# Performance work log

Measured on AMD Instinct MI355X. Metric: run time of the kernel, lower is better.

## Reference

```python
import jax, jax.numpy as jnp
import numpy as np

B, LQ, LKV = 4, 512, 8192
Q_DIM, KV_DIM = 1024, 512
QK_CH, V_CH, N_HEADS = 256, 256, 8
EPS = 1e-5


def _layernorm(x, g, b):
    m = jnp.mean(x, axis=-1, keepdims=True)
    v = jnp.mean(jnp.square(x - m), axis=-1, keepdims=True)
    return (x - m) * jax.lax.rsqrt(v + EPS) * g + b


def setup_inputs() -> dict:
    key = jax.random.key(0)
    ks = jax.random.split(key, 8)
    hidden_states = jax.random.normal(ks[0], (B, LQ, Q_DIM), dtype=jnp.float32)
    inputs = jax.random.normal(ks[1], (B, LKV, KV_DIM), dtype=jnp.float32)
    # Linear weights stored as [in, out] for x @ W
    Wq = jax.random.normal(ks[2], (Q_DIM, QK_CH), dtype=jnp.float32) * (1.0 / np.sqrt(Q_DIM))
    Wk = jax.random.normal(ks[3], (KV_DIM, QK_CH), dtype=jnp.float32) * (1.0 / np.sqrt(KV_DIM))
    Wv = jax.random.normal(ks[4], (KV_DIM, V_CH), dtype=jnp.float32) * (1.0 / np.sqrt(KV_DIM))
    bq = jnp.zeros((QK_CH,), jnp.float32)
    bk = jax.random.normal(ks[5], (QK_CH,), dtype=jnp.float32) * 0.02
    bv = jax.random.normal(ks[6], (V_CH,), dtype=jnp.float32) * 0.02
    ln1_g = jnp.ones((Q_DIM,), jnp.float32)
    ln1_b = jnp.zeros((Q_DIM,), jnp.float32)
    ln2_g = jnp.ones((KV_DIM,), jnp.float32)
    ln2_b = jnp.zeros((KV_DIM,), jnp.float32)
    return dict(hidden_states=hidden_states, inputs=inputs,
                ln1_g=ln1_g, ln1_b=ln1_b, ln2_g=ln2_g, ln2_b=ln2_b,
                Wq=Wq, bq=bq, Wk=Wk, bk=bk, Wv=Wv, bv=bv)


def reference(hidden_states, inputs, ln1_g, ln1_b, ln2_g, ln2_b,
              Wq, bq, Wk, bk, Wv, bv):
    H = N_HEADS
    dqk = QK_CH // H
    dv = V_CH // H
    hs = _layernorm(hidden_states, ln1_g, ln1_b)          # [B,LQ,Q_DIM]
    inp = _layernorm(inputs, ln2_g, ln2_b)                # [B,LKV,KV_DIM]
    q = (hs @ Wq + bq).reshape(B, LQ, H, dqk)             # [B,LQ,H,dqk]
    k = (inp @ Wk + bk).reshape(B, LKV, H, dqk)           # [B,LKV,H,dqk]
    v = (inp @ Wv + bv).reshape(B, LKV, H, dv)            # [B,LKV,H,dv]
    scores = jnp.einsum('bqhd,bkhd->bhqk', q, k) / np.sqrt(dqk).astype(np.float32)
    probs = jax.nn.softmax(scores, axis=-1)               # [B,H,LQ,LKV] (materialized, as in torch)
    ctx = jnp.einsum('bhqk,bkhd->bqhd', probs, v)         # [B,LQ,H,dv]
    return ctx.reshape(B, LQ, H * dv)
```

## Files before the change

kernel.cpp:

```cpp
#include <hip/hip_runtime.h>
#include <hip/hip_bf16.h>
#include <math.h>

#define NB    4
#define LQ    512
#define LKV   8192
#define QDIM  1024
#define KVDIM 512
#define NH    8
#define EPS_LN 1e-5f
#define SMAX  12.0f

typedef __attribute__((ext_vector_type(8))) short bf16x8;
typedef __attribute__((ext_vector_type(4))) float f32x4;

static __device__ __forceinline__ ushort f2bf(float x) {
    unsigned int u = __builtin_bit_cast(unsigned int, x);
    u += 0x7FFFu + ((u >> 16) & 1u);
    return (ushort)(u >> 16);
}

#if __has_builtin(__builtin_amdgcn_cvt_pk_bf16_f32)
static __device__ __forceinline__ unsigned int pk_bf16(float a, float b) {
    auto r = __builtin_amdgcn_cvt_pk_bf16_f32(a, b);
    return __builtin_bit_cast(unsigned int, r);
}
#else
static __device__ __forceinline__ unsigned int pk_bf16(float a, float b) {
    return (unsigned int)f2bf(a) | ((unsigned int)f2bf(b) << 16);
}
#endif

#if __has_builtin(__builtin_amdgcn_exp2f)
#define EXP2F(x) __builtin_amdgcn_exp2f(x)
#else
#define EXP2F(x) exp2f(x)
#endif

static __device__ __forceinline__ void interleave_swap(unsigned int &x, unsigned int &y, int lane) {
#if __has_builtin(__builtin_amdgcn_permlane32_swap) && __has_builtin(__builtin_amdgcn_permlane16_swap)
    {
        auto r1 = __builtin_amdgcn_permlane32_swap(x, y, false, false);
        auto r2 = __builtin_amdgcn_permlane16_swap(r1[0], r1[1], false, false);
        x = (unsigned int)r2[0];
        y = (unsigned int)r2[1];
    }
#else
    {
        unsigned int xs = (unsigned int)__shfl_xor((int)x, 32, 64);
        unsigned int ys = (unsigned int)__shfl_xor((int)y, 32, 64);
        unsigned int A2 = (lane & 32) ? ys : x;
        unsigned int C2 = (lane & 32) ? y  : xs;
        unsigned int A2x = (unsigned int)__shfl_xor((int)A2, 16, 64);
        unsigned int C2x = (unsigned int)__shfl_xor((int)C2, 16, 64);
        x = (lane & 16) ? C2x : A2;
        y = (lane & 16) ? C2  : A2x;
    }
#endif
}

static __device__ __forceinline__ void gld_lds16(const ushort* g, ushort* l) {
    __builtin_amdgcn_global_load_lds(
        (const __attribute__((address_space(1))) unsigned int*)g,
        (__attribute__((address_space(3))) unsigned int*)l, 16, 0, 0);
}

template<int K>
static __device__ __forceinline__ void ln_norm_row(
    const float* __restrict__ x, const float* __restrict__ g,
    const float* __restrict__ bta, ushort* __restrict__ y, int row, int lane)
{
    const float* xp = x + (size_t)row * K;
    constexpr int NV = K / 256;
    float4 v[NV];
    float s = 0.f;
#pragma unroll
    for (int i = 0; i < NV; ++i) {
        v[i] = *(const float4*)(xp + lane * 4 + i * 256);
        s += v[i].x + v[i].y + v[i].z + v[i].w;
    }
#pragma unroll
    for (int o = 1; o < 64; o <<= 1) s += __shfl_xor(s, o, 64);
    const float mu = s * (1.0f / K);
    float vs = 0.f;
#pragma unroll
    for (int i = 0; i < NV; ++i) {
        float dx = v[i].x - mu, dy = v[i].y - mu, dz = v[i].z - mu, dw = v[i].w - mu;
        vs += dx * dx + dy * dy + dz * dz + dw * dw;
    }
#pragma unroll
    for (int o = 1; o < 64; o <<= 1) vs += __shfl_xor(vs, o, 64);
    const float rs = rsqrtf(vs * (1.0f / K) + EPS_LN);
#pragma unroll
    for (int i = 0; i < NV; ++i) {
        const float4 gv = *(const float4*)(g   + lane * 4 + i * 256);
        const float4 bv = *(const float4*)(bta + lane * 4 + i * 256);
        uint2 o;
        o.x = pk_bf16((v[i].x - mu) * rs * gv.x + bv.x, (v[i].y - mu) * rs * gv.y + bv.y);
        o.y = pk_bf16((v[i].z - mu) * rs * gv.z + bv.z, (v[i].w - mu) * rs * gv.w + bv.w);
        *(uint2*)(y + (size_t)row * K + lane * 4 + i * 256) = o;
    }
}

static __device__ __forceinline__ void ln_stats_row(
    const float* __restrict__ x, float* __restrict__ mean, float* __restrict__ rstd,
    int row, int lane)
{
    const float* xp = x + (size_t)row * QDIM;
    float4 v[4];
    float s = 0.f;
#pragma unroll
    for (int i = 0; i < 4; ++i) {
        v[i] = *(const float4*)(xp + lane * 4 + i * 256);
        s += v[i].x + v[i].y + v[i].z + v[i].w;
    }
#pragma unroll
    for (int o = 1; o < 64; o <<= 1) s += __shfl_xor(s, o, 64);
    const float mu = s * (1.0f / QDIM);
    float vs = 0.f;
#pragma unroll
    for (int i = 0; i < 4; ++i) {
        float dx = v[i].x - mu, dy = v[i].y - mu, dz = v[i].z - mu, dw = v[i].w - mu;
        vs += dx * dx + dy * dy + dz * dz + dw * dw;
    }
#pragma unroll
    for (int o = 1; o < 64; o <<= 1) vs += __shfl_xor(vs, o, 64);
    if (lane == 0) {
        mean[row] = mu;
        rstd[row] = rsqrtf(vs * (1.0f / QDIM) + EPS_LN);
    }
}

static __device__ __forceinline__ void wt_transpose_body(
    const float* __restrict__ src, ushort* __restrict__ dst, int K,
    int kx, int ny, int t, ushort (*Ts)[72])
{
    const int k0 = kx * 64, n0 = ny * 64;
    const int nl = t & 63;
#pragma unroll
    for (int p = 0; p < 16; ++p) {
        const int kl = p * 4 + (t >> 6);
        Ts[nl][kl] = f2bf(src[(size_t)(k0 + kl) * 256 + n0 + nl]);
    }
    __syncthreads();
    const int ck = (t & 7) * 8;
#pragma unroll
    for (int p = 0; p < 2; ++p) {
        const int rn = p * 32 + (t >> 3);
        *(bf16x8*)(dst + (size_t)(n0 + rn) * K + k0 + ck) = *(const bf16x8*)&Ts[rn][ck];
    }
}

__global__ __launch_bounds__(256) void phaseA_kernel(
    const float* __restrict__ inputs, const float* __restrict__ ln2g,
    const float* __restrict__ ln2b,   ushort* __restrict__ Abf,
    const float* __restrict__ hidden, float* __restrict__ mean_h, float* __restrict__ rstd_h,
    const float* __restrict__ Wq, const float* __restrict__ Wk, const float* __restrict__ Wv,
    ushort* __restrict__ WtQ, ushort* __restrict__ WtKV)
{
    __shared__ ushort Ts[64][72];
    const int bid = blockIdx.x;
    const int t = threadIdx.x;
    const int lane = t & 63;
    if (bid < 8192) {
        ln_norm_row<KVDIM>(inputs, ln2g, ln2b, Abf, bid * 4 + (t >> 6), lane);
    } else if (bid < 8704) {
        ln_stats_row(hidden, mean_h, rstd_h, (bid - 8192) * 4 + (t >> 6), lane);
    } else if (bid < 8768) {
        const int p = bid - 8704;
        wt_transpose_body(Wq, WtQ, QDIM, p & 15, p >> 4, t, Ts);
    } else if (bid < 8800) {
        const int p = bid - 8768;
        wt_transpose_body(Wk, WtKV, KVDIM, p & 7, p >> 3, t, Ts);
    } else {
        const int p = bid - 8800;
        wt_transpose_body(Wv, WtKV + (size_t)256 * KVDIM, KVDIM, p & 7, p >> 3, t, Ts);
    }
}

__global__ __launch_bounds__(256) void phaseB_kernel(
    const ushort* __restrict__ Abf, const ushort* __restrict__ WtKV,
    const float* __restrict__ bk, const float* __restrict__ bv,
    ushort* __restrict__ kb, ushort* __restrict__ vt,
    const float* __restrict__ hidden, const float* __restrict__ mean_h,
    const float* __restrict__ rstd_h,
    const float* __restrict__ ln1g, const float* __restrict__ ln1b,
    const ushort* __restrict__ WtQ, const float* __restrict__ bq,
    ushort* __restrict__ qb, float oscale)
{
    __shared__ __align__(16) ushort SMEM[4 * 64 * 72];
    const int bid  = blockIdx.x;
    const int t    = threadIdx.x;
    const int lane = t & 63;
    const int w    = t >> 6;
    const int lq   = lane & 15;
    const int lg   = lane >> 4;
    const int wm   = w >> 1;
    const int wn   = w & 1;

    if (bid < 1024) {
        const int bm = (bid >> 2) * 128;
        const int bn = (bid & 3) * 128;
        ushort* As = SMEM;
        ushort* Bs = SMEM + 4096;

        const int srow = t >> 2;
        const int scol = ((t & 3) ^ ((t >> 3) & 3)) * 8;
        const ushort* gA = Abf  + (size_t)(bm + srow) * KVDIM + scol;
        const ushort* gB = WtKV + (size_t)(bn + srow) * KVDIM + scol;
        ushort* lA = As + t * 8;
        ushort* lB = Bs + t * 8;

        f32x4 acc[4][4] = {};
        for (int k0 = 0; k0 < KVDIM; k0 += 32) {
            gld_lds16(gA + k0,                       lA);
            gld_lds16(gA + (size_t)64 * KVDIM + k0,  lA + 2048);
            gld_lds16(gB + k0,                       lB);
            gld_lds16(gB + (size_t)64 * KVDIM + k0,  lB + 2048);
            __syncthreads();
            bf16x8 af[4], bf[4];
#pragma unroll
            for (int mt = 0; mt < 4; ++mt) {
                const int m = wm * 64 + mt * 16 + lq;
                af[mt] = *(const bf16x8*)(As + m * 32 + ((lg ^ ((m >> 1) & 3)) << 3));
            }
#pragma unroll
            for (int nt = 0; nt < 4; ++nt) {
                const int n = wn * 64 + nt * 16 + lq;
                bf[nt] = *(const bf16x8*)(Bs + n * 32 + ((lg ^ ((n >> 1) & 3)) << 3));
            }
#pragma unroll
            for (int mt = 0; mt < 4; ++mt)
#pragma unroll
                for (int nt = 0; nt < 4; ++nt)
                    acc[mt][nt] = __builtin_amdgcn_mfma_f32_16x16x32_bf16(af[mt], bf[nt], acc[mt][nt], 0, 0, 0);
            __syncthreads();
        }
        const int m0base = bm + wm * 64;
        const int bidx   = m0base >> 13;
        const int tokb   = m0base & 8191;

        if (bn < 256) {
            ushort (*Cs)[72] = (ushort(*)[72])(SMEM + w * 64 * 72);
#pragma unroll
            for (int nt = 0; nt < 4; ++nt) {
                const int n_l = nt * 16 + lq;
                const float bias = bk[bn + wn * 64 + n_l];
#pragma unroll
                for (int mt = 0; mt < 4; ++mt)
#pragma unroll
                    for (int r = 0; r < 4; ++r)
                        Cs[mt * 16 + lg * 4 + r][n_l] = f2bf(acc[mt][nt][r] + bias);
            }
            const int r0 = lane >> 3;
            const int ck = (lane & 7) * 8;
            const int nc = bn + wn * 64 + ck;
            const int h = nc >> 5, d = nc & 31;
            const size_t obase = (((size_t)(bidx * NH + h) << 13) + tokb) * 32 + d;
#pragma unroll
            for (int p = 0; p < 8; ++p) {
                const int row = p * 8 + r0;
                *(bf16x8*)(kb + obase + (size_t)row * 32) = *(const bf16x8*)&Cs[row][ck];
            }
        } else {
            ushort (*Cs)[72] = (ushort(*)[72])(SMEM + w * 64 * 72);
#pragma unroll
            for (int nt = 0; nt < 4; ++nt) {
                const int n_l = nt * 16 + lq;
                const float bias = bv[(bn - 256) + wn * 64 + n_l];
#pragma unroll
                for (int mt = 0; mt < 4; ++mt) {
                    uint2 o;
                    o.x = pk_bf16(acc[mt][nt][0] + bias, acc[mt][nt][1] + bias);
                    o.y = pk_bf16(acc[mt][nt][2] + bias, acc[mt][nt][3] + bias);
                    *(uint2*)&Cs[n_l][mt * 16 + lg * 4] = o;
                }
            }
            const int r0 = lane >> 3;
            const int cm = (lane & 7) * 8;
            const int tokc = tokb + cm;
#pragma unroll
            for (int p = 0; p < 8; ++p) {
                const int row = p * 8 + r0;
                const int nv  = (bn - 256) + wn * 64 + row;
                const int h = nv >> 5, d = nv & 31;
                *(bf16x8*)(vt + ((size_t)(bidx * NH + h) * 32 + d) * LKV + tokc) =
                    *(const bf16x8*)&Cs[row][cm];
            }
        }
    } else {
        const int p  = bid - 1024;
        const int bm = (p >> 2) * 64;
        const int bn = (p & 3) * 64;
        ushort* As = SMEM;
        ushort* Bs = SMEM + 4096;

        const int srow = t >> 3;
        const int scol = ((t & 7) ^ (srow & 7)) * 8;
        const ushort* gB = WtQ + (size_t)(bn + srow) * QDIM + scol;
        ushort* lB  = Bs + t * 8;
        ushort* lA0 = As + t * 8;
        ushort* lA1 = As + 2048 + t * 8;

        const int r0 = bm + srow;
        const float mu0 = mean_h[r0],      rs0 = rstd_h[r0];
        const float mu1 = mean_h[r0 + 32], rs1 = rstd_h[r0 + 32];
        const float* xA0 = hidden + (size_t)r0 * QDIM + scol;
        const float* xA1 = xA0 + (size_t)32 * QDIM;

        f32x4 acc[2][2] = {};
        for (int k0 = 0; k0 < QDIM; k0 += 64) {
            gld_lds16(gB + k0,                      lB);
            gld_lds16(gB + (size_t)32 * QDIM + k0,  lB + 2048);
            const float4 a0 = *(const float4*)(xA0 + k0);
            const float4 a1 = *(const float4*)(xA0 + k0 + 4);
            const float4 c0 = *(const float4*)(xA1 + k0);
            const float4 c1 = *(const float4*)(xA1 + k0 + 4);
            const float4 g0 = *(const float4*)(ln1g + k0 + scol);
            const float4 g1 = *(const float4*)(ln1g + k0 + scol + 4);
            const float4 d0 = *(const float4*)(ln1b + k0 + scol);
            const float4 d1 = *(const float4*)(ln1b + k0 + scol + 4);
            uint4 w0, w1;
            w0.x = pk_bf16((a0.x - mu0) * rs0 * g0.x + d0.x, (a0.y - mu0) * rs0 * g0.y + d0.y);
            w0.y = pk_bf16((a0.z - mu0) * rs0 * g0.z + d0.z, (a0.w - mu0) * rs0 * g0.w + d0.w);
            w0.z = pk_bf16((a1.x - mu0) * rs0 * g1.x + d1.x, (a1.y - mu0) * rs0 * g1.y + d1.y);
            w0.w = pk_bf16((a1.z - mu0) * rs0 * g1.z + d1.z, (a1.w - mu0) * rs0 * g1.w + d1.w);
            w1.x = pk_bf16((c0.x - mu1) * rs1 * g0.x + d0.x, (c0.y - mu1) * rs1 * g0.y + d0.y);
            w1.y = pk_bf16((c0.z - mu1) * rs1 * g0.z + d0.z, (c0.w - mu1) * rs1 * g0.w + d0.w);
            w1.z = pk_bf16((c1.x - mu1) * rs1 * g1.x + d1.x, (c1.y - mu1) * rs1 * g1.y + d1.y);
            w1.w = pk_bf16((c1.z - mu1) * rs1 * g1.z + d1.z, (c1.w - mu1) * rs1 * g1.w + d1.w);
            *(uint4*)lA0 = w0;
            *(uint4*)lA1 = w1;
            __syncthreads();
#pragma unroll
            for (int kh = 0; kh < 2; ++kh) {
                bf16x8 af[2], bf[2];
#pragma unroll
                for (int mt = 0; mt < 2; ++mt) {
                    const int m = wm * 32 + mt * 16 + lq;
                    af[mt] = *(const bf16x8*)(As + m * 64 + (((lg + 4 * kh) ^ (m & 7)) << 3));
                }
#pragma unroll
                for (int nt = 0; nt < 2; ++nt) {
                    const int n = wn * 32 + nt * 16 + lq;
                    bf[nt] = *(const bf16x8*)(Bs + n * 64 + (((lg + 4 * kh) ^ (n & 7)) << 3));
                }
#pragma unroll
                for (int mt = 0; mt < 2; ++mt)
#pragma unroll
                    for (int nt = 0; nt < 2; ++nt)
                        acc[mt][nt] = __builtin_amdgcn_mfma_f32_16x16x32_bf16(af[mt], bf[nt], acc[mt][nt], 0, 0, 0);
            }
            __syncthreads();
        }

#pragma unroll
        for (int nt = 0; nt < 2; ++nt) {
            const int n = bn + wn * 32 + nt * 16 + lq;
            const int h = n >> 5, d = n & 31;
            const float bias = bq[n];
#pragma unroll
            for (int mt = 0; mt < 2; ++mt) {
                const int m0   = bm + wm * 32 + mt * 16 + lg * 4;
                const int bidx = m0 >> 9;
                const int tok  = m0 & 511;
                const size_t base = (((size_t)(bidx * NH + h) << 9) + tok) * 32 + d;
#pragma unroll
                for (int r = 0; r < 4; ++r)
                    qb[base + (size_t)r * 32] = f2bf((acc[mt][nt][r] + bias) * oscale);
            }
        }
    }
}

__global__ __launch_bounds__(256, 4) void attn_mfma_kernel(
    const ushort* __restrict__ Qb,
    const ushort* __restrict__ Kb,
    const ushort* __restrict__ Vt,
    float* __restrict__ Opart,
    float* __restrict__ lpart)
{
    const int bid = blockIdx.x;
    const int xcd = bid & 7;
    const int rr  = bid >> 3;
    const int bh  = ((rr & 3) << 3) | xcd;
    const int qt  = (rr >> 2) & 15;
    const int quarter = rr >> 6;
    const int t = threadIdx.x, w = t >> 6, lane = t & 63;
    const int lq = lane & 15, lg = lane >> 4;

    __shared__ __align__(16) float Ob[2 * 32 * 36];
    __shared__ float lbuf[4][32];

    bf16x8 qfrag[2];
    const size_t qbase = ((size_t)bh * LQ + qt * 32) * 32;
    qfrag[0] = *(const bf16x8*)(Qb + qbase + (size_t)lq * 32 + lg * 8);
    qfrag[1] = *(const bf16x8*)(Qb + qbase + (size_t)(16 + lq) * 32 + lg * 8);

    const int kv0 = quarter * 2048 + w * 512;
    const ushort* KpA = Kb + ((size_t)bh * LKV + kv0 + lq) * 32 + lg * 8;
    const ushort* VpA = Vt + ((size_t)bh * 32 + lq) * LKV + kv0 + lg * 8;

    f32x4 oacc[2][2] = {};
    float l_part[2] = {0.f, 0.f};
    const f32x4 cM = {-SMAX, -SMAX, -SMAX, -SMAX};

    bf16x8 kf[4];
#pragma unroll
    for (int m = 0; m < 4; ++m)
        kf[m] = *(const bf16x8*)(KpA + (size_t)(m * 16) * 32);

    for (int kt = 0; kt < 512; kt += 64) {
        bf16x8 kc[4];
#pragma unroll
        for (int m = 0; m < 4; ++m) kc[m] = kf[m];

        bf16x8 vc[2][2];
#pragma unroll
        for (int dt = 0; dt < 2; ++dt)
#pragma unroll
            for (int hf = 0; hf < 2; ++hf)
                vc[dt][hf] = *(const bf16x8*)(VpA + (size_t)(dt * 16) * LKV + kt + hf * 32);

        const int nk = (kt + 64 < 512) ? kt + 64 : 0;
#pragma unroll
        for (int m = 0; m < 4; ++m)
            kf[m] = *(const bf16x8*)(KpA + (size_t)(nk + m * 16) * 32);

        f32x4 s[4][2];
#pragma unroll
        for (int m = 0; m < 4; ++m)
#pragma unroll
            for (int n = 0; n < 2; ++n)
                s[m][n] = __builtin_amdgcn_mfma_f32_16x16x32_bf16(kc[m], qfrag[n], cM, 0, 0, 0);

        bf16x8 pf[2][2];
#pragma unroll
        for (int n = 0; n < 2; ++n) {
#pragma unroll
            for (int z = 0; z < 2; ++z) {
                const float e0 = EXP2F(s[2 * z][n][0]);
                const float e1 = EXP2F(s[2 * z][n][1]);
                const float e2 = EXP2F(s[2 * z][n][2]);
                const float e3 = EXP2F(s[2 * z][n][3]);
                const float f0 = EXP2F(s[2 * z + 1][n][0]);
                const float f1 = EXP2F(s[2 * z + 1][n][1]);
                const float f2 = EXP2F(s[2 * z + 1][n][2]);
                const float f3 = EXP2F(s[2 * z + 1][n][3]);
                l_part[n] += ((e0 + e1) + (e2 + e3)) + ((f0 + f1) + (f2 + f3));
                unsigned int wa = pk_bf16(e0, e1);
                unsigned int wb = pk_bf16(e2, e3);
                unsigned int wc = pk_bf16(f0, f1);
                unsigned int wd = pk_bf16(f2, f3);
                interleave_swap(wa, wc, lane);
                interleave_swap(wb, wd, lane);
                uint4 wv;
                wv.x = wa; wv.y = wb; wv.z = wc; wv.w = wd;
                pf[n][z] = __builtin_bit_cast(bf16x8, wv);
            }
        }

#pragma unroll
        for (int dt = 0; dt < 2; ++dt)
#pragma unroll
            for (int n = 0; n < 2; ++n) {
                oacc[dt][n] = __builtin_amdgcn_mfma_f32_16x16x32_bf16(vc[dt][0], pf[n][0], oacc[dt][n], 0, 0, 0);
                oacc[dt][n] = __builtin_amdgcn_mfma_f32_16x16x32_bf16(vc[dt][1], pf[n][1], oacc[dt][n], 0, 0, 0);
            }
    }

#pragma unroll
    for (int n = 0; n < 2; ++n) {
        l_part[n] += __shfl_xor(l_part[n], 16);
        l_part[n] += __shfl_xor(l_part[n], 32);
    }
    if (lg == 0) {
        lbuf[w][lq]      = l_part[0];
        lbuf[w][16 + lq] = l_part[1];
    }
    if (w >= 2) {
#pragma unroll
        for (int n = 0; n < 2; ++n)
#pragma unroll
            for (int dt = 0; dt < 2; ++dt)
                *(f32x4*)&Ob[((size_t)(w - 2) * 32 + n * 16 + lq) * 36 + dt * 16 + lg * 4] = oacc[dt][n];
    }
    __syncthreads();
    if (w < 2) {
#pragma unroll
        for (int n = 0; n < 2; ++n)
#pragma unroll
            for (int dt = 0; dt < 2; ++dt) {
                float* p = &Ob[((size_t)w * 32 + n * 16 + lq) * 36 + dt * 16 + lg * 4];
                f32x4 v = *(f32x4*)p;
                v += oacc[dt][n];
                *(f32x4*)p = v;
            }
    }
    __syncthreads();
    {
        const int pidx = (quarter * 32 + bh) * 16 + qt;
        const int q  = t >> 3;
        const int d0 = (t & 7) * 4;
        f32x4 s0 = *(const f32x4*)&Ob[((size_t)q) * 36 + d0];
        f32x4 s1 = *(const f32x4*)&Ob[((size_t)(32 + q)) * 36 + d0];
        s0 += s1;
        *(f32x4*)(Opart + (size_t)pidx * 1024 + q * 32 + d0) = s0;
        if ((t & 7) == 0) {
            float gl = lbuf[0][q] + lbuf[1][q] + lbuf[2][q] + lbuf[3][q];
            lpart[(size_t)pidx * 32 + q] = gl;
        }
    }
}

__global__ __launch_bounds__(256) void attn_combine_kernel(
    const float* __restrict__ Opart, const float* __restrict__ lpart,
    float* __restrict__ Out)
{
    const int cb = blockIdx.x;
    const int bh = cb >> 4, qt = cb & 15;
    const int b = bh >> 3, h = bh & 7;
    const int t = threadIdx.x;
    const int q = t >> 3;
    const int dq = (t & 7) * 4;
    float4 o = {0.f, 0.f, 0.f, 0.f};
    float l = 0.f;
#pragma unroll
    for (int j = 0; j < 4; ++j) {
        const size_t pidx = (size_t)((j * 32 + bh) * 16 + qt);
        const float4 a = *(const float4*)(Opart + pidx * 1024 + q * 32 + dq);
        o.x += a.x; o.y += a.y; o.z += a.z; o.w += a.w;
        l += lpart[pidx * 32 + q];
    }
    const float inv = 1.0f / l;
    o.x *= inv; o.y *= inv; o.z *= inv; o.w *= inv;
    *(float4*)(Out + ((size_t)b * LQ + qt * 32 + q) * 256 + h * 32 + dq) = o;
}

extern "C" void kernel_launch(void* const* d_in, const int* in_sizes, int n_in,
                              void* d_out, int out_size, void* d_ws, size_t ws_size,
                              hipStream_t stream)
{
    const float* hidden = (const float*)d_in[0];
    const float* inputs = (const float*)d_in[1];
    const float* ln1g   = (const float*)d_in[2];
    const float* ln1b   = (const float*)d_in[3];
    const float* ln2g   = (const float*)d_in[4];
    const float* ln2b   = (const float*)d_in[5];
    const float* Wq     = (const float*)d_in[6];
    const float* bq     = (const float*)d_in[7];
    const float* Wk     = (const float*)d_in[8];
    const float* bk     = (const float*)d_in[9];
    const float* Wv     = (const float*)d_in[10];
    const float* bv     = (const float*)d_in[11];
    float* out = (float*)d_out;

    char* wsb = (char*)d_ws;
    ushort* qb     = (ushort*)(wsb);
    ushort* WtKV   = (ushort*)(wsb + (1u << 20));
    ushort* WtQ    = (ushort*)(wsb + (1u << 20) + (512u << 10));
    float*  mean_h = (float*)(wsb + (2u << 20));
    float*  rstd_h = (float*)(wsb + (2u << 20) + 8192);
    ushort* kb     = (ushort*)(wsb + (2u << 20) + 16384);
    ushort* vt     = (ushort*)(wsb + (18u << 20) + 16384);
    ushort* Abf    = (ushort*)(wsb + (34u << 20) + 16384);

    float* Opart = (float*)Abf;
    float* lpart = Opart + (size_t)4 * 32 * 16 * 1024;

    const float oscale = 0.2550540226496112f;

    phaseA_kernel<<<8832, 256, 0, stream>>>(inputs, ln2g, ln2b, Abf,
                                            hidden, mean_h, rstd_h,
                                            Wq, Wk, Wv, WtQ, WtKV);
    phaseB_kernel<<<1152, 256, 0, stream>>>(Abf, WtKV, bk, bv, kb, vt,
                                            hidden, mean_h, rstd_h, ln1g, ln1b,
                                            WtQ, bq, qb, oscale);
    attn_mfma_kernel<<<2048, 256, 0, stream>>>(qb, kb, vt, Opart, lpart);
    attn_combine_kernel<<<512, 256, 0, stream>>>(Opart, lpart, out);
}
```

Baseline: 219.0 us.

## Double K-step of KV projection GEMM and reorder attention block mapping

The KV projection GEMM now loads a 64-wide K slice per iteration instead of 32, halving the number of loop iterations and barrier pairs. It uses an 8-way XOR swizzle adapted to the 64-element row stride. Separately, the attention kernel's block-index decode is reordered so consecutive blocks on an XCD share the same batch-head, which should improve L2 locality for K/V. The price is doubled LDS use for the GEMM tiles, which could lower occupancy.

```diff
diff --git a/kernel.cpp b/kernel.cpp
--- a/kernel.cpp
+++ b/kernel.cpp
@@ -202,38 +202,40 @@
         const int bm = (bid >> 2) * 128;
         const int bn = (bid & 3) * 128;
         ushort* As = SMEM;
-        ushort* Bs = SMEM + 4096;
-
-        const int srow = t >> 2;
-        const int scol = ((t & 3) ^ ((t >> 3) & 3)) * 8;
+        ushort* Bs = SMEM + 8192;
+
+        const int srow = t >> 3;
+        const int scol = ((t & 7) ^ (srow & 7)) * 8;
         const ushort* gA = Abf  + (size_t)(bm + srow) * KVDIM + scol;
         const ushort* gB = WtKV + (size_t)(bn + srow) * KVDIM + scol;
-        ushort* lA = As + t * 8;
-        ushort* lB = Bs + t * 8;
 
         f32x4 acc[4][4] = {};
-        for (int k0 = 0; k0 < KVDIM; k0 += 32) {
-            gld_lds16(gA + k0,                       lA);
-            gld_lds16(gA + (size_t)64 * KVDIM + k0,  lA + 2048);
-            gld_lds16(gB + k0,                       lB);
-            gld_lds16(gB + (size_t)64 * KVDIM + k0,  lB + 2048);
+        for (int k0 = 0; k0 < KVDIM; k0 += 64) {
+#pragma unroll
+            for (int p = 0; p < 4; ++p) {
+                gld_lds16(gA + (size_t)(p * 32) * KVDIM + k0, As + p * 2048 + t * 8);
+                gld_lds16(gB + (size_t)(p * 32) * KVDIM + k0, Bs + p * 2048 + t * 8);
+            }
             __syncthreads();
-            bf16x8 af[4], bf[4];
-#pragma unroll
-            for (int mt = 0; mt < 4; ++mt) {
-                const int m = wm * 64 + mt * 16 + lq;
-                af[mt] = *(const bf16x8*)(As + m * 32 + ((lg ^ ((m >> 1) & 3)) << 3));
-            }
-#pragma unroll
-            for (int nt = 0; nt < 4; ++nt) {
-                const int n = wn * 64 + nt * 16 + lq;
-                bf[nt] = *(const bf16x8*)(Bs + n * 32 + ((lg ^ ((n >> 1) & 3)) << 3));
-            }
-#pragma unroll
-            for (int mt = 0; mt < 4; ++mt)
-#pragma unroll
-                for (int nt = 0; nt < 4; ++nt)
-                    acc[mt][nt] = __builtin_amdgcn_mfma_f32_16x16x32_bf16(af[mt], bf[nt], acc[mt][nt], 0, 0, 0);
+#pragma unroll
+            for (int kh = 0; kh < 2; ++kh) {
+                bf16x8 af[4], bf[4];
+#pragma unroll
+                for (int mt = 0; mt < 4; ++mt) {
+                    const int m = wm * 64 + mt * 16 + lq;
+                    af[mt] = *(const bf16x8*)(As + m * 64 + (((lg + 4 * kh) ^ (m & 7)) << 3));
+                }
+#pragma unroll
+                for (int nt = 0; nt < 4; ++nt) {
+                    const int n = wn * 64 + nt * 16 + lq;
+                    bf[nt] = *(const bf16x8*)(Bs + n * 64 + (((lg + 4 * kh) ^ (n & 7)) << 3));
+                }
+#pragma unroll
+                for (int mt = 0; mt < 4; ++mt)
+#pragma unroll
+                    for (int nt = 0; nt < 4; ++nt)
+                        acc[mt][nt] = __builtin_amdgcn_mfma_f32_16x16x32_bf16(af[mt], bf[nt], acc[mt][nt], 0, 0, 0);
+            }
             __syncthreads();
         }
         const int m0base = bm + wm * 64;
@@ -382,10 +384,12 @@
 {
     const int bid = blockIdx.x;
     const int xcd = bid & 7;
-    const int rr  = bid >> 3;
-    const int bh  = ((rr & 3) << 3) | xcd;
-    const int qt  = (rr >> 2) & 15;
-    const int quarter = rr >> 6;
+    const int u   = bid >> 3;
+    const int bhw = u >> 6;
+    const int r2  = u & 63;
+    const int qt  = r2 >> 2;
+    const int quarter = r2 & 3;
+    const int bh  = (bhw << 3) | xcd;
     const int t = threadIdx.x, w = t >> 6, lane = t & 63;
     const int lq = lane & 15, lg = lane >> 4;
 
```

New measurement: 215.8 us. No clear change (-1.4%).
